# Kernel tuning notes

Measured on AMD Instinct MI355X. Metric: run time of the kernel, lower is better.

The kernel has to match this reference:

```python
import jax, jax.numpy as jnp
import numpy as np

B, N, R, DIM = 4, 1024, 5, 1024
H, DH = 16, 64
ALPHA = 128.0
# FLAGS.fix_attention=True, a_sim=False: q * (dim_head**-0.5 * alpha**-1) * mult**-0.5
SCALE = (DH ** -0.5) * (1.0 / ALPHA) * (R ** -0.5)
EPS = 1e-5


def layernorm(x, g):
    mean = jnp.mean(x, axis=-1, keepdims=True)
    var = jnp.mean((x - mean) ** 2, axis=-1, keepdims=True)  # unbiased=False
    return (x - mean) * jax.lax.rsqrt(var + EPS) * g


def setup_inputs() -> dict:
    key = jax.random.key(0)
    ks = jax.random.split(key, 8)
    x = jax.random.normal(ks[0], (B, N, R, DIM), dtype=jnp.float32)
    mask = jax.random.bernoulli(ks[1], 0.9, (B, N))
    g_in = jnp.ones((DIM,), dtype=jnp.float32)
    Wq = jax.random.normal(ks[2], (DIM, H * DH), dtype=jnp.float32) * 0.02
    Wkv = jax.random.normal(ks[3], (DIM, 2 * DH), dtype=jnp.float32) * 0.02
    null_kv = jax.random.normal(ks[4], (2, DH), dtype=jnp.float32)
    Wout = jax.random.normal(ks[5], (H * DH, DIM), dtype=jnp.float32) * 0.02
    g_out = jnp.ones((DIM,), dtype=jnp.float32)
    return {"x": x, "mask": mask, "g_in": g_in, "Wq": Wq, "Wkv": Wkv,
            "null_kv": null_kv, "Wout": Wout, "g_out": g_out}


def reference(x, mask, g_in, Wq, Wkv, null_kv, Wout, g_out):
    # context defaults to the UN-normalized x (set before norm in the original)
    context = x
    xn = layernorm(x, g_in)                               # [b,n,r,dim]
    q = jnp.einsum('bnrc,ce->bnre', xn, Wq)               # [b,n,r,h*d]
    q = q.reshape(B, N, R, H, DH).transpose(0, 3, 1, 2, 4)  # b h n r d
    q = q * SCALE
    kv = jnp.einsum('bnrc,ce->bnre', context, Wkv)        # [b,n,r,2d] (multi-query: 1 kv head)
    k, v = kv[..., :DH], kv[..., DH:]                     # [b,n,r,d]
    # null kv token prepended along the j (sequence) axis, repeated over r
    nk = jnp.broadcast_to(null_kv[0], (B, 1, R, DH))
    nv = jnp.broadcast_to(null_kv[1], (B, 1, R, DH))
    k = jnp.concatenate([nk, k], axis=1)                  # [b,n+1,r,d]
    v = jnp.concatenate([nv, v], axis=1)
    sim = jnp.einsum('bhird,bjrd->bhij', q, k)            # [b,h,n,n+1]
    big = jnp.finfo(sim.dtype).max
    maskp = jnp.pad(mask, ((0, 0), (1, 0)), constant_values=True)  # null token always visible
    sim = jnp.where(maskp[:, None, None, :], sim, -big)
    # pb-relax: subtract detached row max, rescale by alpha
    sim = sim - jax.lax.stop_gradient(jnp.max(sim, axis=-1, keepdims=True))
    attn = jax.nn.softmax(sim * ALPHA, axis=-1)
    out = jnp.einsum('bhij,bjrd->bhird', attn, v)         # b h n r d
    out = out.transpose(0, 2, 3, 1, 4).reshape(B, N, R, H * DH)
    out = jnp.einsum('bnre,eo->bnro', out, Wout)
    return layernorm(out, g_out)
```

## Files before the change

kernel.cpp:

```cpp
#include <hip/hip_runtime.h>

#define B_   4
#define N_   1024
#define R_   5
#define DIM_ 1024
#define H_   16
#define DH_  64
#define NJ   1056
#define CDIM 320
#define MROWS (B_*N_*R_)

typedef unsigned int u32;
typedef unsigned short u16;
typedef __attribute__((ext_vector_type(8))) short bf16x8;
typedef __attribute__((ext_vector_type(4))) float f32x4;
typedef __attribute__((ext_vector_type(16))) float f32x16;

constexpr float SCALEA_ = 0.05590169943749474f;

__device__ __forceinline__ u16 f2bf(float f) {
  u32 u = __builtin_bit_cast(u32, f);
  u32 r = (u + 0x7fffu + ((u >> 16) & 1u)) >> 16;
  return (u16)r;
}
__device__ __forceinline__ u32 pack2(float lo, float hi) {
  return (u32)f2bf(lo) | ((u32)f2bf(hi) << 16);
}
__device__ __forceinline__ void gld_lds16(void* lds, const void* g) {
  __builtin_amdgcn_global_load_lds((const __attribute__((address_space(1))) u32*)g,
                                   (__attribute__((address_space(3))) u32*)lds, 16, 0, 0);
}

__global__ void mask_detect(const u32* __restrict__ m, int* __restrict__ flag) {
  int t = threadIdx.x;
  int fl = 0;
  for (int i = t; i < 1024; i += 256) {
    u32 wv = m[i];
    if (wv == 0x3f800000u) fl |= 4;
    else if (wv > 1u) fl |= 2;
    if ((i & 1) && wv == 1u) fl |= 1;
  }
  if (fl) atomicOr(flag, fl);
}

__global__ void build_bias(const void* __restrict__ mask, const int* __restrict__ flag,
                           float* __restrict__ biasg) {
  int idx = blockIdx.x * 256 + threadIdx.x;
  if (idx >= B_ * NJ) return;
  int b = idx / NJ, j = idx % NJ;
  int mv;
  if (j == 0) mv = 1;
  else if (j > N_) mv = 0;
  else {
    int fb = flag[0];
    int mode = (fb & 4) ? 2 : ((fb & 2) ? 1 : ((fb & 1) ? 0 : 3));
    int mi = b * N_ + (j - 1);
    if (mode == 0)      mv = ((const int*)mask)[mi] != 0;
    else if (mode == 1) mv = ((const unsigned char*)mask)[mi] != 0;
    else if (mode == 2) mv = ((const float*)mask)[mi] != 0.0f;
    else                mv = ((const int*)mask)[mi * 2] != 0;
  }
  biasg[idx] = mv ? 0.0f : -__builtin_inff();
}

__global__ void kvfill(const float* __restrict__ nullkv, u16* __restrict__ kg, u16* __restrict__ vTg) {
  int idx = blockIdx.x * 256 + threadIdx.x;
  if (idx >= B_ * 32 * CDIM) return;
  int c  = idx % CDIM;
  int jj = (idx / CDIM) & 31;
  int b  = idx / (CDIM * 32);
  int j  = (jj == 0) ? 0 : (1024 + jj);
  u16 kvv, vvv;
  if (jj == 0) { kvv = f2bf(nullkv[c & 63]); vvv = f2bf(nullkv[64 + (c & 63)]); }
  else         { kvv = 0; vvv = 0; }
  kg [(size_t)(b * NJ + j) * CDIM + c] = kvv;
  vTg[(((size_t)b * 33 + (j >> 5)) * CDIM + c) * 32 + (j & 31)] = vvv;
}

__global__ __launch_bounds__(256) void transpose_cast(const float* __restrict__ W,
                                                      u16* __restrict__ WT, int K, int Nn) {
  __shared__ float tile[32][33];
  int tx = threadIdx.x & 31, ty = threadIdx.x >> 5;
  int n0 = blockIdx.x * 32, k0 = blockIdx.y * 32;
  #pragma unroll
  for (int e = 0; e < 4; ++e)
    tile[ty + e * 8][tx] = W[(size_t)(k0 + ty + e * 8) * Nn + n0 + tx];
  __syncthreads();
  #pragma unroll
  for (int e = 0; e < 4; ++e)
    WT[(size_t)(n0 + ty + e * 8) * K + k0 + tx] = f2bf(tile[tx][ty + e * 8]);
}

__global__ __launch_bounds__(256) void ln_in(const float* __restrict__ x, const float* __restrict__ gin,
                                             u16* __restrict__ xn, u16* __restrict__ xb) {
  const size_t row = blockIdx.x;
  const int t = threadIdx.x, w = t >> 6, lane = t & 63;
  const float* xr = x + row * 1024;
  f32x4 v = *(const f32x4*)(xr + t * 4);
  float s = v[0] + v[1] + v[2] + v[3];
  #pragma unroll
  for (int o = 1; o < 64; o <<= 1) s += __shfl_xor(s, o);
  __shared__ float red[8];
  if (lane == 0) red[w] = s;
  __syncthreads();
  float mean = (red[0] + red[1] + red[2] + red[3]) * (1.0f / 1024.0f);
  f32x4 d;
  float ss = 0.f;
  #pragma unroll
  for (int e = 0; e < 4; ++e) { d[e] = v[e] - mean; ss += d[e] * d[e]; }
  #pragma unroll
  for (int o = 1; o < 64; o <<= 1) ss += __shfl_xor(ss, o);
  if (lane == 0) red[4 + w] = ss;
  __syncthreads();
  float var = (red[4] + red[5] + red[6] + red[7]) * (1.0f / 1024.0f);
  float rs = rsqrtf(var + 1e-5f);
  f32x4 gv = *(const f32x4*)(gin + t * 4);
  uint2 o1, o2;
  o1.x = pack2(d[0] * rs * gv[0], d[1] * rs * gv[1]);
  o1.y = pack2(d[2] * rs * gv[2], d[3] * rs * gv[3]);
  o2.x = pack2(v[0], v[1]);
  o2.y = pack2(v[2], v[3]);
  *(uint2*)(xn + row * 1024 + t * 4) = o1;
  *(uint2*)(xb + row * 1024 + t * 4) = o2;
}

__global__ __launch_bounds__(256) void ln_out(float* __restrict__ y, const float* __restrict__ gout) {
  const size_t row = blockIdx.x;
  const int t = threadIdx.x, w = t >> 6, lane = t & 63;
  float* yr = y + row * 1024;
  f32x4 v = *(const f32x4*)(yr + t * 4);
  float s = v[0] + v[1] + v[2] + v[3];
  #pragma unroll
  for (int o = 1; o < 64; o <<= 1) s += __shfl_xor(s, o);
  __shared__ float red[8];
  if (lane == 0) red[w] = s;
  __syncthreads();
  float mean = (red[0] + red[1] + red[2] + red[3]) * (1.0f / 1024.0f);
  f32x4 d;
  float ss = 0.f;
  #pragma unroll
  for (int e = 0; e < 4; ++e) { d[e] = v[e] - mean; ss += d[e] * d[e]; }
  #pragma unroll
  for (int o = 1; o < 64; o <<= 1) ss += __shfl_xor(ss, o);
  if (lane == 0) red[4 + w] = ss;
  __syncthreads();
  float var = (red[4] + red[5] + red[6] + red[7]) * (1.0f / 1024.0f);
  float rs = rsqrtf(var + 1e-5f);
  f32x4 gv = *(const f32x4*)(gout + t * 4);
  f32x4 o;
  #pragma unroll
  for (int e = 0; e < 4; ++e) o[e] = d[e] * rs * gv[e];
  *(f32x4*)(yr + t * 4) = o;
}

template <int EPI>
__global__ __launch_bounds__(256) void gemm_bt(const u16* __restrict__ A, const u16* __restrict__ BT,
                                               void* __restrict__ C0, void* __restrict__ C1,
                                               const int K, const int Nn) {
  __shared__ __align__(16) u16 As[128 * 32];
  __shared__ __align__(16) u16 Bs[128 * 32];
  const int t = threadIdx.x, w = t >> 6, lane = t & 63;
  const int g = lane >> 4, i16 = lane & 15;
  const int wr = w >> 1, wc = w & 1;
  const size_t m0 = (size_t)blockIdx.y * 128;
  const size_t n0 = (size_t)blockIdx.x * 128;
  const u16* Ab = A + m0 * K;
  const u16* Bb = BT + n0 * K;
  f32x4 acc[4][4];
  #pragma unroll
  for (int mi = 0; mi < 4; ++mi)
    #pragma unroll
    for (int ni = 0; ni < 4; ++ni) acc[mi][ni] = (f32x4){0.f, 0.f, 0.f, 0.f};

  for (int k0 = 0; k0 < K; k0 += 32) {
    __syncthreads();
    #pragma unroll
    for (int s = 0; s < 2; ++s) {
      int c = s * 256 + t;
      gld_lds16(&As[(s * 256 + w * 64) * 8], Ab + (size_t)(c >> 2) * K + k0 + (c & 3) * 8);
      gld_lds16(&Bs[(s * 256 + w * 64) * 8], Bb + (size_t)(c >> 2) * K + k0 + (c & 3) * 8);
    }
    __syncthreads();
    bf16x8 af[4], bfr[4];
    #pragma unroll
    for (int mi = 0; mi < 4; ++mi) af[mi]  = *(const bf16x8*)&As[(wr * 64 + mi * 16 + i16) * 32 + g * 8];
    #pragma unroll
    for (int ni = 0; ni < 4; ++ni) bfr[ni] = *(const bf16x8*)&Bs[(wc * 64 + ni * 16 + i16) * 32 + g * 8];
    #pragma unroll
    for (int mi = 0; mi < 4; ++mi)
      #pragma unroll
      for (int ni = 0; ni < 4; ++ni)
        acc[mi][ni] = __builtin_amdgcn_mfma_f32_16x16x32_bf16(af[mi], bfr[ni], acc[mi][ni], 0, 0, 0);
  }

  #pragma unroll
  for (int mi = 0; mi < 4; ++mi)
    #pragma unroll
    for (int ni = 0; ni < 4; ++ni)
      #pragma unroll
      for (int reg = 0; reg < 4; ++reg) {
        size_t gr = m0 + wr * 64 + mi * 16 + g * 4 + reg;
        int gc = (int)n0 + wc * 64 + ni * 16 + i16;
        float v = acc[mi][ni][reg];
        if (EPI == 0) {
          ((u16*)C0)[gr * 1024 + gc] = f2bf(v * SCALEA_);
        } else if (EPI == 1) {
          int grr = (int)gr;
          int b = grr / (N_ * R_);
          int rem = grr - b * (N_ * R_);
          int n = rem / R_;
          int r = rem - n * R_;
          int j = n + 1;
          u16 val = f2bf(v);
          if (gc < DH_) ((u16*)C0)[(size_t)(b * NJ + j) * CDIM + r * 64 + gc] = val;
          else ((u16*)C1)[(((size_t)b * 33 + (j >> 5)) * CDIM + r * 64 + (gc - DH_)) * 32 + (j & 31)] = val;
        } else {
          ((float*)C0)[gr * 1024 + gc] = v;
        }
      }
}

__global__ __launch_bounds__(256, 2) void attn_kernel(const u16* __restrict__ qb, const u16* __restrict__ kg,
                                                      const u16* __restrict__ vTg, const float* __restrict__ biasg,
                                                      u16* __restrict__ attout) {
  const int blk0 = blockIdx.x;
  const int blk = (blk0 & 7) * 128 + (blk0 >> 3);
  const int ch = blk & 1;
  const int it = (blk >> 1) & 7;
  const int h  = (blk >> 4) & 15;
  const int b  = blk >> 8;
  const int t = threadIdx.x;
  const int w = t >> 6, lane = t & 63;
  const int l31 = lane & 31, lh = lane >> 5;
  const int i0 = it * 128 + w * 32;

  __shared__ __align__(16) char Kl[2][20480];
  __shared__ __align__(16) char Vl[10240];

  int ksrc[5];
  #pragma unroll
  for (int s = 0; s < 5; ++s) {
    int d = w * 320 + s * 64 + lane;
    int j = d / 40, c16 = d - j * 40;
    int fj = (j & 7) ^ (j >> 3);
    ksrc[s] = j * 640 + ((c16 ^ fj) << 4);
  }
  int vsrc[3];
  #pragma unroll
  for (int s = 0; s < 3; ++s) {
    int d = s * 256 + t;
    int vc = d >> 2, sl = d & 3;
    int gv = (vc & 3) ^ ((vc >> 3) & 3);
    vsrc[s] = (ch * 160 + vc) * 64 + ((sl ^ gv) << 4);
  }
  const char* ktile = (const char*)(kg + (size_t)b * NJ * CDIM);
  const char* vtile = (const char*)(vTg + (size_t)b * 33 * CDIM * 32);

  bf16x8 qf[20];
  {
    const u16* qrow = qb + ((size_t)(b * N_ + i0 + l31) * R_) * 1024 + h * 64 + lh * 8;
    #pragma unroll
    for (int kk = 0; kk < 20; ++kk) {
      int k16 = kk * 16;
      qf[kk] = *(const bf16x8*)(qrow + (k16 >> 6) * 1024 + (k16 & 63));
    }
  }

  const float* bptr = biasg + b * NJ + lh * 4;

  f32x16 O[5];
  #pragma unroll
  for (int cf = 0; cf < 5; ++cf)
    #pragma unroll
    for (int r = 0; r < 16; ++r) O[cf][r] = 0.f;
  float d_run = 0.f;

  #pragma unroll
  for (int s = 0; s < 5; ++s)
    gld_lds16(&Kl[0][w * 5120 + s * 1024], ktile + ksrc[s]);

  const int swzK = ((l31 & 7) ^ (l31 >> 3)) << 4;
  const int swzV = ((l31 & 3) ^ ((l31 >> 3) & 3)) << 4;

  for (int jt = 0; jt < 33; ++jt) {
    const int cur = jt & 1;

    asm volatile("s_waitcnt vmcnt(0)" ::: "memory");
    __builtin_amdgcn_s_barrier();
    __builtin_amdgcn_sched_barrier(0);

    {
      const char* vt = vtile + (size_t)jt * 20480;
      gld_lds16(&Vl[w * 1024],        vt + vsrc[0]);
      gld_lds16(&Vl[4096 + w * 1024], vt + vsrc[1]);
      if (w < 2) gld_lds16(&Vl[8192 + w * 1024], vt + vsrc[2]);
    }
    if (jt < 32) {
      const char* kt1 = ktile + (size_t)(jt + 1) * 20480;
      #pragma unroll
      for (int s = 0; s < 5; ++s)
        gld_lds16(&Kl[cur ^ 1][w * 5120 + s * 1024], kt1 + ksrc[s]);
    }

    const char* Kb  = &Kl[cur][0] + l31 * 640;
    const char* kb0 = Kb + ((0x00 | (lh << 4)) ^ swzK);
    const char* kb1 = Kb + ((0x20 | (lh << 4)) ^ swzK);
    const char* kb2 = Kb + ((0x40 | (lh << 4)) ^ swzK);
    const char* kb3 = Kb + ((0x60 | (lh << 4)) ^ swzK);
    f32x16 S0, S1;
    #pragma unroll
    for (int r = 0; r < 16; ++r) { S0[r] = 0.f; S1[r] = 0.f; }
    __builtin_amdgcn_s_setprio(1);
    #pragma unroll
    for (int kk = 0; kk < 20; ++kk) {
      const char* kb = ((kk & 3) == 0) ? kb0 : ((kk & 3) == 1) ? kb1 : ((kk & 3) == 2) ? kb2 : kb3;
      bf16x8 kf = *(const bf16x8*)(kb + (kk >> 2) * 128);
      if (kk & 1) S1 = __builtin_amdgcn_mfma_f32_32x32x16_bf16(kf, qf[kk], S1, 0, 0, 0);
      else        S0 = __builtin_amdgcn_mfma_f32_32x32x16_bf16(kf, qf[kk], S0, 0, 0, 0);
    }
    __builtin_amdgcn_s_setprio(0);

    f32x4 bb0 = *(const f32x4*)(bptr + (size_t)jt * 32 + 0);
    f32x4 bb1 = *(const f32x4*)(bptr + (size_t)jt * 32 + 8);
    f32x4 bb2 = *(const f32x4*)(bptr + (size_t)jt * 32 + 16);
    f32x4 bb3 = *(const f32x4*)(bptr + (size_t)jt * 32 + 24);
    float p[16];
    float ts = 0.f;
    #pragma unroll
    for (int r = 0; r < 16; ++r) {
      float bv = (r < 4) ? bb0[r & 3] : (r < 8) ? bb1[r & 3] : (r < 12) ? bb2[r & 3] : bb3[r & 3];
      float L = fminf(S0[r] + S1[r] + bv, 60.0f);
      p[r] = __expf(L);
      ts += p[r];
    }
    d_run += ts;

    u32 pk0 = pack2(p[0], p[1]),   pk1 = pack2(p[2], p[3]);
    u32 pk2 = pack2(p[4], p[5]),   pk3 = pack2(p[6], p[7]);
    u32 pk4 = pack2(p[8], p[9]),   pk5 = pack2(p[10], p[11]);
    u32 pk6 = pack2(p[12], p[13]), pk7 = pack2(p[14], p[15]);
    asm volatile("v_permlane32_swap_b32 %0, %1" : "+v"(pk0), "+v"(pk2));
    asm volatile("v_permlane32_swap_b32 %0, %1" : "+v"(pk1), "+v"(pk3));
    asm volatile("v_permlane32_swap_b32 %0, %1" : "+v"(pk4), "+v"(pk6));
    asm volatile("v_permlane32_swap_b32 %0, %1" : "+v"(pk5), "+v"(pk7));
    union { u32 u[4]; bf16x8 v; } f1, f2;
    f1.u[0] = pk0; f1.u[1] = pk1; f1.u[2] = pk2; f1.u[3] = pk3;
    f2.u[0] = pk4; f2.u[1] = pk5; f2.u[2] = pk6; f2.u[3] = pk7;

    if (jt < 32) asm volatile("s_waitcnt vmcnt(5)" ::: "memory");
    else         asm volatile("s_waitcnt vmcnt(0)" ::: "memory");
    __builtin_amdgcn_s_barrier();
    __builtin_amdgcn_sched_barrier(0);

    const char* Vb  = &Vl[0] + l31 * 64;
    const char* vb1 = Vb + ((lh << 4) ^ swzV);
    const char* vb2 = Vb + (((lh ^ 2) << 4) ^ swzV);
    __builtin_amdgcn_s_setprio(1);
    #pragma unroll
    for (int cf = 0; cf < 5; ++cf) {
      bf16x8 v0 = *(const bf16x8*)(vb1 + cf * 2048);
      bf16x8 v1 = *(const bf16x8*)(vb2 + cf * 2048);
      O[cf] = __builtin_amdgcn_mfma_f32_32x32x16_bf16(f1.v, v0, O[cf], 0, 0, 0);
      O[cf] = __builtin_amdgcn_mfma_f32_32x32x16_bf16(f2.v, v1, O[cf], 0, 0, 0);
    }
    __builtin_amdgcn_s_setprio(0);
  }

  d_run += __shfl_xor(d_run, 32);
  float inv = 1.0f / d_run;
  float invr[16];
  #pragma unroll
  for (int r = 0; r < 16; ++r) invr[r] = __shfl(inv, (r & 3) + 8 * (r >> 2) + 4 * lh);

  #pragma unroll
  for (int r = 0; r < 16; ++r) {
    int gi = i0 + (r & 3) + 8 * (r >> 2) + 4 * lh;
    u16* orow = attout + ((size_t)(b * N_ + gi) * R_) * 1024 + h * 64;
    #pragma unroll
    for (int cf = 0; cf < 5; ++cf) {
      int c = ch * 160 + cf * 32 + l31;
      orow[(c >> 6) * 1024 + (c & 63)] = f2bf(O[cf][r] * invr[r]);
    }
  }
}

extern "C" void kernel_launch(void* const* d_in, const int* in_sizes, int n_in,
                              void* d_out, int out_size, void* d_ws, size_t ws_size,
                              hipStream_t stream) {
  (void)in_sizes; (void)n_in; (void)out_size; (void)ws_size;
  const float* x      = (const float*)d_in[0];
  const void*  mask   = d_in[1];
  const float* g_in   = (const float*)d_in[2];
  const float* Wq     = (const float*)d_in[3];
  const float* Wkv    = (const float*)d_in[4];
  const float* nullkv = (const float*)d_in[5];
  const float* Wout   = (const float*)d_in[6];
  const float* g_out  = (const float*)d_in[7];
  float* out = (float*)d_out;

  char* base = (char*)d_ws;
  size_t off = 0;
  auto carve = [&](size_t bytes) { char* r = base + off; off += (bytes + 255) & ~(size_t)255; return r; };
  int*   flag  = (int*)carve(4);
  float* biasg = (float*)carve((size_t)B_ * NJ * 4);
  u16* WqT   = (u16*)carve((size_t)1024 * 1024 * 2);
  u16* WkvT  = (u16*)carve((size_t)128 * 1024 * 2);
  u16* WoutT = (u16*)carve((size_t)1024 * 1024 * 2);
  u16* xn    = (u16*)carve((size_t)MROWS * 1024 * 2);
  u16* xb    = (u16*)carve((size_t)MROWS * 1024 * 2);
  u16* qb    = (u16*)carve((size_t)MROWS * 1024 * 2);
  u16* kg    = (u16*)carve((size_t)B_ * NJ * CDIM * 2);
  u16* vTg   = (u16*)carve((size_t)B_ * 33 * CDIM * 32 * 2);
  u16* attout = xn;

  hipMemsetAsync(flag, 0, 4, stream);
  mask_detect<<<1, 256, 0, stream>>>((const u32*)mask, flag);
  build_bias<<<(B_ * NJ + 255) / 256, 256, 0, stream>>>(mask, flag, biasg);
  kvfill<<<(B_ * 32 * CDIM + 255) / 256, 256, 0, stream>>>(nullkv, kg, vTg);
  transpose_cast<<<dim3(32, 32), 256, 0, stream>>>(Wq, WqT, 1024, 1024);
  transpose_cast<<<dim3(4, 32), 256, 0, stream>>>(Wkv, WkvT, 1024, 128);
  transpose_cast<<<dim3(32, 32), 256, 0, stream>>>(Wout, WoutT, 1024, 1024);
  ln_in<<<MROWS, 256, 0, stream>>>(x, g_in, xn, xb);
  gemm_bt<0><<<dim3(8, 160), 256, 0, stream>>>(xn, WqT, qb, nullptr, 1024, 1024);
  gemm_bt<1><<<dim3(1, 160), 256, 0, stream>>>(xb, WkvT, kg, vTg, 1024, 128);
  attn_kernel<<<1024, 256, 0, stream>>>(qb, kg, vTg, biasg, attout);
  gemm_bt<2><<<dim3(8, 160), 256, 0, stream>>>(attout, WoutT, out, nullptr, 1024, 1024);
  ln_out<<<MROWS, 256, 0, stream>>>(out, g_out);
}
```

Before: 437.8 us.

## Double-buffer V tiles, fold log2e into Q scale, bf16 output intermediate

The attention kernel now double-buffers V in LDS alongside K, prefetching the next V tile together with the next K tile. This removes the mid-iteration wait and barrier before the PV MFMAs. The log2(e) factor is folded into the Q scale so exp2f replaces __expf, the clamp is adjusted to match, and P is packed with the hardware v_cvt_pk_bf16_f32 instruction instead of software rounding. The output projection GEMM now writes bf16 instead of fp32, and a separate ln_out reads it and writes the final fp32 result, which halves intermediate traffic at some precision cost before the final layernorm.

Measured after the change: 428.7 us. 2.1% less time.

```diff
diff --git a/kernel.cpp b/kernel.cpp
--- a/kernel.cpp
+++ b/kernel.cpp
@@ -16,7 +16,7 @@
 typedef __attribute__((ext_vector_type(4))) float f32x4;
 typedef __attribute__((ext_vector_type(16))) float f32x16;
 
-constexpr float SCALEA_ = 0.05590169943749474f;
+constexpr float SCALEA_ = (float)(0.05590169943749474 * 1.4426950408889634);
 
 __device__ __forceinline__ u16 f2bf(float f) {
   u32 u = __builtin_bit_cast(u32, f);
@@ -124,11 +124,16 @@
   *(uint2*)(xb + row * 1024 + t * 4) = o2;
 }
 
-__global__ __launch_bounds__(256) void ln_out(float* __restrict__ y, const float* __restrict__ gout) {
+__global__ __launch_bounds__(256) void ln_out(const u16* __restrict__ yb, const float* __restrict__ gout,
+                                              float* __restrict__ out) {
   const size_t row = blockIdx.x;
   const int t = threadIdx.x, w = t >> 6, lane = t & 63;
-  float* yr = y + row * 1024;
-  f32x4 v = *(const f32x4*)(yr + t * 4);
+  uint2 raw = *(const uint2*)(yb + row * 1024 + t * 4);
+  f32x4 v;
+  v[0] = __builtin_bit_cast(float, (raw.x & 0xffffu) << 16);
+  v[1] = __builtin_bit_cast(float, (raw.x & 0xffff0000u));
+  v[2] = __builtin_bit_cast(float, (raw.y & 0xffffu) << 16);
+  v[3] = __builtin_bit_cast(float, (raw.y & 0xffff0000u));
   float s = v[0] + v[1] + v[2] + v[3];
   #pragma unroll
   for (int o = 1; o < 64; o <<= 1) s += __shfl_xor(s, o);
@@ -150,7 +155,7 @@
   f32x4 o;
   #pragma unroll
   for (int e = 0; e < 4; ++e) o[e] = d[e] * rs * gv[e];
-  *(f32x4*)(yr + t * 4) = o;
+  *(f32x4*)(out + row * 1024 + t * 4) = o;
 }
 
 template <int EPI>
@@ -215,7 +220,7 @@
           if (gc < DH_) ((u16*)C0)[(size_t)(b * NJ + j) * CDIM + r * 64 + gc] = val;
           else ((u16*)C1)[(((size_t)b * 33 + (j >> 5)) * CDIM + r * 64 + (gc - DH_)) * 32 + (j & 31)] = val;
         } else {
-          ((float*)C0)[gr * 1024 + gc] = v;
+          ((u16*)C0)[gr * 1024 + gc] = f2bf(v);
         }
       }
 }
@@ -235,7 +240,7 @@
   const int i0 = it * 128 + w * 32;
 
   __shared__ __align__(16) char Kl[2][20480];
-  __shared__ __align__(16) char Vl[10240];
+  __shared__ __align__(16) char Vl[2][10240];
 
   int ksrc[5];
   #pragma unroll
@@ -278,6 +283,11 @@
   #pragma unroll
   for (int s = 0; s < 5; ++s)
     gld_lds16(&Kl[0][w * 5120 + s * 1024], ktile + ksrc[s]);
+  {
+    gld_lds16(&Vl[0][w * 1024],        vtile + vsrc[0]);
+    gld_lds16(&Vl[0][4096 + w * 1024], vtile + vsrc[1]);
+    if (w < 2) gld_lds16(&Vl[0][8192 + w * 1024], vtile + vsrc[2]);
+  }
 
   const int swzK = ((l31 & 7) ^ (l31 >> 3)) << 4;
   const int swzV = ((l31 & 3) ^ ((l31 >> 3) & 3)) << 4;
@@ -289,17 +299,15 @@
     __builtin_amdgcn_s_barrier();
     __builtin_amdgcn_sched_barrier(0);
 
-    {
-      const char* vt = vtile + (size_t)jt * 20480;
-      gld_lds16(&Vl[w * 1024],        vt + vsrc[0]);
-      gld_lds16(&Vl[4096 + w * 1024], vt + vsrc[1]);
-      if (w < 2) gld_lds16(&Vl[8192 + w * 1024], vt + vsrc[2]);
-    }
     if (jt < 32) {
       const char* kt1 = ktile + (size_t)(jt + 1) * 20480;
+      const char* vt1 = vtile + (size_t)(jt + 1) * 20480;
       #pragma unroll
       for (int s = 0; s < 5; ++s)
         gld_lds16(&Kl[cur ^ 1][w * 5120 + s * 1024], kt1 + ksrc[s]);
+      gld_lds16(&Vl[cur ^ 1][w * 1024],        vt1 + vsrc[0]);
+      gld_lds16(&Vl[cur ^ 1][4096 + w * 1024], vt1 + vsrc[1]);
+      if (w < 2) gld_lds16(&Vl[cur ^ 1][8192 + w * 1024], vt1 + vsrc[2]);
     }
 
     const char* Kb  = &Kl[cur][0] + l31 * 640;
@@ -329,16 +337,21 @@
     #pragma unroll
     for (int r = 0; r < 16; ++r) {
       float bv = (r < 4) ? bb0[r & 3] : (r < 8) ? bb1[r & 3] : (r < 12) ? bb2[r & 3] : bb3[r & 3];
-      float L = fminf(S0[r] + S1[r] + bv, 60.0f);
-      p[r] = __expf(L);
+      float L = fminf(S0[r] + S1[r] + bv, 80.0f);
+      p[r] = exp2f(L);
       ts += p[r];
     }
     d_run += ts;
 
-    u32 pk0 = pack2(p[0], p[1]),   pk1 = pack2(p[2], p[3]);
-    u32 pk2 = pack2(p[4], p[5]),   pk3 = pack2(p[6], p[7]);
-    u32 pk4 = pack2(p[8], p[9]),   pk5 = pack2(p[10], p[11]);
-    u32 pk6 = pack2(p[12], p[13]), pk7 = pack2(p[14], p[15]);
+    u32 pk0, pk1, pk2, pk3, pk4, pk5, pk6, pk7;
+    asm("v_cvt_pk_bf16_f32 %0, %1, %2" : "=v"(pk0) : "v"(p[0]),  "v"(p[1]));
+    asm("v_cvt_pk_bf16_f32 %0, %1, %2" : "=v"(pk1) : "v"(p[2]),  "v"(p[3]));
+    asm("v_cvt_pk_bf16_f32 %0, %1, %2" : "=v"(pk2) : "v"(p[4]),  "v"(p[5]));
+    asm("v_cvt_pk_bf16_f32 %0, %1, %2" : "=v"(pk3) : "v"(p[6]),  "v"(p[7]));
+    asm("v_cvt_pk_bf16_f32 %0, %1, %2" : "=v"(pk4) : "v"(p[8]),  "v"(p[9]));
+    asm("v_cvt_pk_bf16_f32 %0, %1, %2" : "=v"(pk5) : "v"(p[10]), "v"(p[11]));
+    asm("v_cvt_pk_bf16_f32 %0, %1, %2" : "=v"(pk6) : "v"(p[12]), "v"(p[13]));
+    asm("v_cvt_pk_bf16_f32 %0, %1, %2" : "=v"(pk7) : "v"(p[14]), "v"(p[15]));
     asm volatile("v_permlane32_swap_b32 %0, %1" : "+v"(pk0), "+v"(pk2));
     asm volatile("v_permlane32_swap_b32 %0, %1" : "+v"(pk1), "+v"(pk3));
     asm volatile("v_permlane32_swap_b32 %0, %1" : "+v"(pk4), "+v"(pk6));
@@ -347,12 +360,7 @@
     f1.u[0] = pk0; f1.u[1] = pk1; f1.u[2] = pk2; f1.u[3] = pk3;
     f2.u[0] = pk4; f2.u[1] = pk5; f2.u[2] = pk6; f2.u[3] = pk7;
 
-    if (jt < 32) asm volatile("s_waitcnt vmcnt(5)" ::: "memory");
-    else         asm volatile("s_waitcnt vmcnt(0)" ::: "memory");
-    __builtin_amdgcn_s_barrier();
-    __builtin_amdgcn_sched_barrier(0);
-
-    const char* Vb  = &Vl[0] + l31 * 64;
+    const char* Vb  = &Vl[cur][0] + l31 * 64;
     const char* vb1 = Vb + ((lh << 4) ^ swzV);
     const char* vb2 = Vb + (((lh ^ 2) << 4) ^ swzV);
     __builtin_amdgcn_s_setprio(1);
@@ -412,6 +420,7 @@
   u16* kg    = (u16*)carve((size_t)B_ * NJ * CDIM * 2);
   u16* vTg   = (u16*)carve((size_t)B_ * 33 * CDIM * 32 * 2);
   u16* attout = xn;
+  u16* yb     = xb;
 
   hipMemsetAsync(flag, 0, 4, stream);
   mask_detect<<<1, 256, 0, stream>>>((const u32*)mask, flag);
@@ -424,6 +433,6 @@
   gemm_bt<0><<<dim3(8, 160), 256, 0, stream>>>(xn, WqT, qb, nullptr, 1024, 1024);
   gemm_bt<1><<<dim3(1, 160), 256, 0, stream>>>(xb, WkvT, kg, vTg, 1024, 128);
   attn_kernel<<<1024, 256, 0, stream>>>(qb, kg, vTg, biasg, attout);
-  gemm_bt<2><<<dim3(8, 160), 256, 0, stream>>>(attout, WoutT, out, nullptr, 1024, 1024);
-  ln_out<<<MROWS, 256, 0, stream>>>(out, g_out);
-}
+  gemm_bt<2><<<dim3(8, 160), 256, 0, stream>>>(attout, WoutT, yb, nullptr, 1024, 1024);
+  ln_out<<<MROWS, 256, 0, stream>>>(yb, g_out, out);
+}
```
